# Performance work log

Hardware: AMD Instinct MI355X
Metric: run time of the kernel (lower is better)

The kernel has to match this reference:

```python
import jax, jax.numpy as jnp
import numpy as np


def setup_inputs() -> dict:
    key = jax.random.key(0)
    ks = jax.random.split(key, 5)
    B, D, W = 8, 768, 128
    scale = 1.0 / np.sqrt(D)
    return {
        "x": jax.random.normal(ks[0], (B, D, W, W), dtype=jnp.float32),
        "in_proj_w": jax.random.normal(ks[1], (3 * D, D), dtype=jnp.float32) * scale,
        "in_proj_b": jax.random.normal(ks[2], (3 * D,), dtype=jnp.float32) * 0.01,
        "out_w": jax.random.normal(ks[3], (D, D), dtype=jnp.float32) * scale,
        "out_b": jax.random.normal(ks[4], (D,), dtype=jnp.float32) * 0.01,
        "num_heads": 12,
        "num_tokens": 8,
    }


def reference(x, in_proj_w, in_proj_b, out_w, out_b, num_heads, num_tokens):
    B, D, Wd, Hd = x.shape
    nt = num_tokens
    gs = Hd // nt            # grid (block) size
    T = nt * nt              # number of blocks / queries
    S = gs * gs              # k/v tokens per block
    h = num_heads
    hd = D // h

    # ---- query: adaptive avg pool to (nt, nt), flatten, permute -> (B, T, D)
    q = x.reshape(B, D, nt, gs, nt, gs).mean(axis=(3, 5))      # (B, D, nt, nt)
    q = q.reshape(B, D, T).transpose(0, 2, 1)                   # (B, T, D)

    # ---- key/value: faithful reproduction of unfold + view(x.size()) + reshape
    # torch: kv_perm (B,W,H,D) -> unfold -> (B, nt, nt, D, gs, gs) contiguous,
    # then reinterpreted flat as (B, W*H, D) (scrambles channel/pixel layout).
    t = x.transpose(0, 2, 3, 1)                                 # (B, W, H, D)
    t = t.reshape(B, nt, gs, nt, gs, D).transpose(0, 1, 3, 5, 2, 4)  # (B,nt,nt,D,gs,gs)
    kv = t.reshape(B, T, S, D)                                  # chunked into T blocks of S tokens

    # ---- in-projections (torch MultiheadAttention packed weights)
    Wq, Wk, Wv = in_proj_w[:D], in_proj_w[D:2 * D], in_proj_w[2 * D:]
    bq, bk, bv = in_proj_b[:D], in_proj_b[D:2 * D], in_proj_b[2 * D:]
    qp = (q @ Wq.T + bq).reshape(B, T, h, hd)                   # (B, T, h, hd)
    kp = (kv @ Wk.T + bk).reshape(B, T, S, h, hd)               # (B, T, S, h, hd)
    vp = (kv @ Wv.T + bv).reshape(B, T, S, h, hd)

    # ---- block-local single-query attention, batched over all T blocks
    scores = jnp.einsum("bthd,btshd->bths", qp, kp) / np.sqrt(hd)  # (B, T, h, S)
    attn = jax.nn.softmax(scores, axis=-1)
    ctx = jnp.einsum("bths,btshd->bthd", attn, vp).reshape(B, T, D)

    # ---- out projection
    return ctx @ out_w.T + out_b                                # (B, T, D)
```

## Files before the change

kernel.cpp:

```cpp
#include <hip/hip_runtime.h>
#include <hip/hip_bf16.h>

#define D_ 768
#define W_ 128
#define T_ 64
#define S_ 256
#define H_ 12
#define HH_ 6
#define BT_ 512

__device__ __forceinline__ unsigned short f2bf(float f) {
  unsigned u = __float_as_uint(f);
  u = (u + 0x7FFFu + ((u >> 16) & 1u)) >> 16;
  return (unsigned short)u;
}
__device__ __forceinline__ float bfu(unsigned s) {
  return __uint_as_float(s << 16);
}

__global__ __launch_bounds__(384) void k_pack(const float* __restrict__ x,
                                              unsigned short* __restrict__ packed,
                                              float* __restrict__ q) {
  const int blk  = blockIdx.x;
  const int cc   = blk & 15;
  const int tjp  = (blk >> 4) & 3;
  const int ti   = (blk >> 6) & 7;
  const int b    = blk >> 9;
  const int tid  = threadIdx.x;
  const int c8   = tid & 7;
  const int ch   = tid >> 3;
  const int btl  = c8 >> 2;
  const int btg0 = b*64 + ti*8 + tjp*2;
  const int ch0  = cc * 48;

  __shared__ unsigned short tile[48][2][260];
  __shared__ float poolsc[48][2];

  const float* xcol = x + (size_t)b*D_*16384 + (size_t)(ch0 + ch)*16384
                        + (16*ti)*128 + 32*tjp + c8*4;

  float psum = 0.f;
  #pragma unroll
  for (int r = 0; r < 16; ++r) {
    const float4 v = *(const float4*)(xcol + r*128);
    const int px = r*16 + (c8 & 3)*4;
    unsigned lo = (unsigned)f2bf(v.x) | ((unsigned)f2bf(v.y) << 16);
    unsigned hi = (unsigned)f2bf(v.z) | ((unsigned)f2bf(v.w) << 16);
    *(uint2*)&tile[ch][btl][px] = make_uint2(lo, hi);
    psum += (v.x + v.y) + (v.z + v.w);
  }
  psum += __shfl_xor(psum, 1);
  psum += __shfl_xor(psum, 2);
  if ((c8 & 3) == 0) poolsc[ch][btl] = psum;
  __syncthreads();

  for (int ii = tid; ii < 512; ii += 384) {
    const int bl = ii >> 8, p = ii & 255;
    unsigned short* pbt = packed + ((size_t)(btg0 + bl)*16 + cc)*D_*16;
    #pragma unroll
    for (int c = 0; c < 3; ++c) {
      unsigned u[8];
      #pragma unroll
      for (int k2 = 0; k2 < 8; ++k2) {
        const unsigned a  = tile[3*(2*k2)     + c][bl][p];
        const unsigned b2 = tile[3*(2*k2 + 1) + c][bl][p];
        u[k2] = a | (b2 << 16);
      }
      unsigned short* dst = pbt + (size_t)(c*256 + p)*16;
      *(uint4*)(dst)     = make_uint4(u[0], u[1], u[2], u[3]);
      *(uint4*)(dst + 8) = make_uint4(u[4], u[5], u[6], u[7]);
    }
  }
  if (tid < 96) {
    const int ch2 = tid >> 1, bl = tid & 1;
    q[(size_t)(btg0 + bl)*D_ + ch0 + ch2] = poolsc[ch2][bl] * (1.0f/256.0f);
  }
}

__global__ __launch_bounds__(256) void k_qp(const float* __restrict__ q,
                                            const float* __restrict__ ipw,
                                            const float* __restrict__ ipb,
                                            float* __restrict__ qp) {
  const int jt = blockIdx.x >> 5;
  const int bt0 = (blockIdx.x & 31) * 16;
  const int tid = threadIdx.x;
  const float* Wr = ipw + (size_t)jt*64*D_;
  __shared__ float wt[64][65];
  __shared__ float at[16][65];
  const int i = tid & 63, qw = tid >> 6;
  float acc[4] = {0,0,0,0};
  for (int dc = 0; dc < D_; dc += 64) {
    #pragma unroll
    for (int k = 0; k < 4; ++k) {
      const int idx = k*256 + tid;
      const int r = idx >> 4, c4 = idx & 15;
      *(float4*)&wt[r][c4*4] = *(const float4*)(Wr + (size_t)r*D_ + dc + c4*4);
    }
    {
      const int r = tid >> 4, c4 = tid & 15;
      *(float4*)&at[r][c4*4] = *(const float4*)(q + (size_t)(bt0 + r)*D_ + dc + c4*4);
    }
    __syncthreads();
    #pragma unroll
    for (int dd = 0; dd < 64; ++dd) {
      const float wv = wt[i][dd];
      #pragma unroll
      for (int k = 0; k < 4; ++k)
        acc[k] += at[qw + k*4][dd] * wv;
    }
    __syncthreads();
  }
  const float bqv = ipb[jt*64 + i];
  #pragma unroll
  for (int k = 0; k < 4; ++k)
    qp[(size_t)(bt0 + qw + k*4)*D_ + jt*64 + i] = acc[k] + bqv;
}

__global__ __launch_bounds__(256) void k_fold(const float* __restrict__ qp,
                                              const float* __restrict__ ipw,
                                              unsigned short* __restrict__ qkout) {
  const int btc = blockIdx.x & 15;
  const int nt  = blockIdx.x >> 4;
  const int h   = nt / 12;
  const int ddc = (nt % 12) * 64;
  const int bt0 = btc * 32;
  const int tid = threadIdx.x;
  __shared__ float qpl[32][68];
  __shared__ float wkl[64][68];
  #pragma unroll
  for (int k = 0; k < 2; ++k) {
    const int idx = k*256 + tid;
    const int r = idx >> 4, c4 = idx & 15;
    *(float4*)&qpl[r][c4*4] = *(const float4*)(qp + (size_t)(bt0 + r)*D_ + h*64 + c4*4);
  }
  #pragma unroll
  for (int k = 0; k < 4; ++k) {
    const int idx = k*256 + tid;
    const int r = idx >> 4, c4 = idx & 15;
    *(float4*)&wkl[r][c4*4] = *(const float4*)(ipw + (size_t)(D_ + h*64 + r)*D_ + ddc + c4*4);
  }
  __syncthreads();
  const int i = tid & 63, qw = tid >> 6;
  float acc[8] = {0,0,0,0,0,0,0,0};
  #pragma unroll 8
  for (int kk = 0; kk < 64; ++kk) {
    const float w = wkl[kk][i];
    #pragma unroll
    for (int k = 0; k < 8; ++k)
      acc[k] += qpl[qw + k*4][kk] * w;
  }
  #pragma unroll
  for (int k = 0; k < 8; ++k)
    qkout[((size_t)(bt0 + qw + k*4)*H_ + h)*D_ + ddc + i] = f2bf(acc[k] * 0.125f);
}

__global__ __launch_bounds__(256) void k_attn3(const unsigned short* __restrict__ packed,
                                               const unsigned short* __restrict__ qkin,
                                               float* __restrict__ wout) {
  const int hg = blockIdx.x >> 9;
  const int bt = blockIdx.x & 511;
  const int tid = threadIdx.x;
  const int wv = tid >> 6, lane = tid & 63;
  __shared__ float pool_lds[HH_ * D_];
  __shared__ float sc[HH_][S_];

  {
    const uint4* src = (const uint4*)(qkin + ((size_t)bt*H_ + hg*HH_)*D_);
    #pragma unroll
    for (int k = 0; k < 3; ++k) {
      const int idx = k*256 + tid;
      if (idx < 576) {
        const uint4 v = src[idx];
        float* d = pool_lds + idx*8;
        d[0] = bfu(v.x & 0xFFFFu); d[1] = bfu(v.x >> 16);
        d[2] = bfu(v.y & 0xFFFFu); d[3] = bfu(v.y >> 16);
        d[4] = bfu(v.z & 0xFFFFu); d[5] = bfu(v.z >> 16);
        d[6] = bfu(v.w & 0xFFFFu); d[7] = bfu(v.w >> 16);
      }
    }
  }
  __syncthreads();

  float acc[HH_][4];
  #pragma unroll
  for (int h = 0; h < HH_; ++h)
    #pragma unroll
    for (int j = 0; j < 4; ++j) acc[h][j] = 0.f;

  {
    const unsigned short* pb = packed + ((size_t)bt*16 + (lane >> 2))*D_*16 + (lane & 3)*4;
    const int d0 = wv * 192;
    #pragma unroll 4
    for (int d4 = 0; d4 < 48; ++d4) {
      const int d = d0 + d4*4;
      float f[4][4];
      #pragma unroll
      for (int dd = 0; dd < 4; ++dd) {
        const short4 pv = *(const short4*)(pb + (size_t)(d + dd)*16);
        f[dd][0] = bfu((unsigned)(unsigned short)pv.x);
        f[dd][1] = bfu((unsigned)(unsigned short)pv.y);
        f[dd][2] = bfu((unsigned)(unsigned short)pv.z);
        f[dd][3] = bfu((unsigned)(unsigned short)pv.w);
      }
      #pragma unroll
      for (int h = 0; h < HH_; ++h) {
        const float4 qv = *(const float4*)&pool_lds[h*D_ + d];
        #pragma unroll
        for (int j = 0; j < 4; ++j)
          acc[h][j] += qv.x*f[0][j] + qv.y*f[1][j] + qv.z*f[2][j] + qv.w*f[3][j];
      }
    }
  }
  __syncthreads();

  if (wv == 0) {
    #pragma unroll
    for (int h = 0; h < HH_; ++h)
      *(float4*)&sc[h][lane*4] = make_float4(acc[h][0], acc[h][1], acc[h][2], acc[h][3]);
  } else {
    float* dstp = pool_lds + (size_t)(wv - 1)*(HH_*S_);
    #pragma unroll
    for (int h = 0; h < HH_; ++h)
      *(float4*)&dstp[h*S_ + lane*4] = make_float4(acc[h][0], acc[h][1], acc[h][2], acc[h][3]);
  }
  __syncthreads();
  #pragma unroll
  for (int h = 0; h < HH_; ++h)
    sc[h][tid] += pool_lds[0*(HH_*S_) + h*S_ + tid]
                + pool_lds[1*(HH_*S_) + h*S_ + tid]
                + pool_lds[2*(HH_*S_) + h*S_ + tid];
  __syncthreads();

  if (wv < 3) {
    #pragma unroll
    for (int hh = 0; hh < 2; ++hh) {
      const int h = wv*2 + hh;
      float4 v = *(const float4*)(&sc[h][lane*4]);
      float m = fmaxf(fmaxf(v.x, v.y), fmaxf(v.z, v.w));
      #pragma unroll
      for (int off = 32; off > 0; off >>= 1) m = fmaxf(m, __shfl_xor(m, off));
      const float e0 = __expf(v.x - m), e1 = __expf(v.y - m),
                  e2 = __expf(v.z - m), e3 = __expf(v.w - m);
      float ss = (e0+e1)+(e2+e3);
      #pragma unroll
      for (int off = 32; off > 0; off >>= 1) ss += __shfl_xor(ss, off);
      const float inv = 1.0f / ss;
      *(float4*)(&sc[h][lane*4]) = make_float4(e0*inv, e1*inv, e2*inv, e3*inv);
    }
  }
  __syncthreads();

  float wacc[HH_][3];
  #pragma unroll
  for (int h = 0; h < HH_; ++h) { wacc[h][0]=0.f; wacc[h][1]=0.f; wacc[h][2]=0.f; }
  const unsigned short* prow = packed + (size_t)bt*16*D_*16;
  #pragma unroll 2
  for (int s8 = 0; s8 < 32; ++s8) {
    float f[3][8];
    #pragma unroll
    for (int c = 0; c < 3; ++c) {
      const uint4 pv = *(const uint4*)(prow + ((size_t)(s8 >> 1)*D_ + c*256 + tid)*16
                                            + (s8 & 1)*8);
      f[c][0] = bfu(pv.x & 0xFFFFu); f[c][1] = bfu(pv.x >> 16);
      f[c][2] = bfu(pv.y & 0xFFFFu); f[c][3] = bfu(pv.y >> 16);
      f[c][4] = bfu(pv.z & 0xFFFFu); f[c][5] = bfu(pv.z >> 16);
      f[c][6] = bfu(pv.w & 0xFFFFu); f[c][7] = bfu(pv.w >> 16);
    }
    #pragma unroll
    for (int h = 0; h < HH_; ++h) {
      const float4 a0 = *(const float4*)&sc[h][s8*8];
      const float4 a1 = *(const float4*)&sc[h][s8*8 + 4];
      #pragma unroll
      for (int c = 0; c < 3; ++c)
        wacc[h][c] += a0.x*f[c][0] + a0.y*f[c][1] + a0.z*f[c][2] + a0.w*f[c][3]
                    + a1.x*f[c][4] + a1.y*f[c][5] + a1.z*f[c][6] + a1.w*f[c][7];
    }
  }
  float* wp = wout + ((size_t)bt*H_ + hg*HH_)*D_;
  #pragma unroll
  for (int h = 0; h < HH_; ++h)
    #pragma unroll
    for (int c = 0; c < 3; ++c)
      wp[h*D_ + c*256 + tid] = wacc[h][c];
}

__global__ __launch_bounds__(256) void k_q(const float* __restrict__ x, float* __restrict__ q) {
  const int bd = blockIdx.x;
  const int tid = threadIdx.x;
  const float4* xp = (const float4*)(x + (size_t)bd * (W_*W_));
  float acc[8] = {0,0,0,0,0,0,0,0};
  #pragma unroll
  for (int k = 0; k < 16; ++k) {
    float4 v = xp[k*256 + tid];
    acc[k>>1] += (v.x + v.y) + (v.z + v.w);
  }
  __shared__ float part[256][9];
  #pragma unroll
  for (int i = 0; i < 8; ++i) part[tid][i] = acc[i];
  __syncthreads();
  if (tid < 64) {
    const int ti = tid >> 3, tj = tid & 7;
    float s = 0.f;
    #pragma unroll
    for (int m = 0; m < 8; ++m)
      #pragma unroll
      for (int n = 0; n < 4; ++n)
        s += part[m*32 + tj*4 + n][ti];
    const int b = bd / D_, d = bd - b*D_;
    q[(size_t)(b*T_ + tid)*D_ + d] = s * (1.0f/256.0f);
  }
}

__global__ __launch_bounds__(256) void k_attn(const float* __restrict__ x,
                                              const unsigned short* __restrict__ qkin,
                                              float* __restrict__ wout) {
  const int bt = blockIdx.x;
  const int b = bt >> 6, t = bt & 63;
  const int ti = t >> 3, tj = t & 7;
  const int tid = threadIdx.x;
  __shared__ float qkl[H_*D_];
  __shared__ float sc[H_][S_];
  const float* xb = x + (size_t)b*D_*W_*W_ + ti*16*W_ + tj*16;
  {
    const uint4* src = (const uint4*)(qkin + (size_t)bt*H_*D_);
    #pragma unroll
    for (int k = 0; k < 5; ++k) {
      const int idx = k*256 + tid;
      if (idx < 1152) {
        const uint4 v = src[idx];
        float* d = qkl + idx*8;
        d[0] = bfu(v.x & 0xFFFFu); d[1] = bfu(v.x >> 16);
        d[2] = bfu(v.y & 0xFFFFu); d[3] = bfu(v.y >> 16);
        d[4] = bfu(v.z & 0xFFFFu); d[5] = bfu(v.z >> 16);
        d[6] = bfu(v.w & 0xFFFFu); d[7] = bfu(v.w >> 16);
      }
    }
  }
  __syncthreads();
  float acc[H_];
  #pragma unroll
  for (int h = 0; h < H_; ++h) acc[h] = 0.f;
  #pragma unroll
  for (int c = 0; c < 3; ++c) {
    const float* chp = xb + (size_t)(3*tid + c)*(W_*W_);
    for (int blk = 0; blk < 8; ++blk) {
      float4 v[8];
      #pragma unroll
      for (int u = 0; u < 8; ++u) {
        const int pg = blk*8 + u;
        v[u] = *(const float4*)(chp + (pg>>2)*W_ + (pg&3)*4);
      }
      const int dbase = c*256 + blk*32;
      #pragma unroll
      for (int h = 0; h < H_; ++h) {
        const float4* qh = (const float4*)(qkl + h*D_ + dbase);
        float s0 = 0.f;
        #pragma unroll
        for (int u = 0; u < 8; ++u) {
          const float4 qq = qh[u];
          s0 += qq.x*v[u].x + qq.y*v[u].y + qq.z*v[u].z + qq.w*v[u].w;
        }
        acc[h] += s0;
      }
    }
  }
  #pragma unroll
  for (int h = 0; h < H_; ++h) sc[h][tid] = acc[h];
  __syncthreads();
  {
    const int wv = tid >> 6, lane = tid & 63;
    #pragma unroll
    for (int hh = 0; hh < 3; ++hh) {
      const int h = wv*3 + hh;
      float4 v = *(const float4*)(&sc[h][lane*4]);
      float m = fmaxf(fmaxf(v.x, v.y), fmaxf(v.z, v.w));
      #pragma unroll
      for (int off = 32; off > 0; off >>= 1) m = fmaxf(m, __shfl_xor(m, off));
      const float e0 = __expf(v.x - m), e1 = __expf(v.y - m),
                  e2 = __expf(v.z - m), e3 = __expf(v.w - m);
      float ss = (e0+e1)+(e2+e3);
      #pragma unroll
      for (int off = 32; off > 0; off >>= 1) ss += __shfl_xor(ss, off);
      const float inv = 1.0f / ss;
      *(float4*)(&sc[h][lane*4]) = make_float4(e0*inv, e1*inv, e2*inv, e3*inv);
    }
  }
  __syncthreads();
  float wacc[H_][3];
  #pragma unroll
  for (int h = 0; h < H_; ++h) { wacc[h][0]=0.f; wacc[h][1]=0.f; wacc[h][2]=0.f; }
  const float* xp0 = xb + (tid>>4)*W_ + (tid&15);
  for (int s = 0; s < S_; ++s) {
    const float p0 = xp0[(size_t)(3*s+0)*(W_*W_)];
    const float p1 = xp0[(size_t)(3*s+1)*(W_*W_)];
    const float p2 = xp0[(size_t)(3*s+2)*(W_*W_)];
    #pragma unroll
    for (int h = 0; h < H_; ++h) {
      const float at = sc[h][s];
      wacc[h][0] += at*p0; wacc[h][1] += at*p1; wacc[h][2] += at*p2;
    }
  }
  float* wp = wout + (size_t)bt*H_*D_;
  #pragma unroll
  for (int h = 0; h < H_; ++h)
    #pragma unroll
    for (int c = 0; c < 3; ++c)
      wp[h*D_ + c*256 + tid] = wacc[h][c];
}

__global__ __launch_bounds__(256) void k_ctx(const float* __restrict__ wbuf,
                                             const float* __restrict__ ipw,
                                             const float* __restrict__ ipb,
                                             float* __restrict__ ctx) {
  const int h = blockIdx.x >> 5;
  const int bt0 = (blockIdx.x & 31) * 16;
  const int tid = threadIdx.x;
  const float* Wv = ipw + (size_t)2*D_*D_ + (size_t)h*64*D_;
  __shared__ float wt[64][65];
  __shared__ float at[16][65];
  const int i = tid & 63, qw = tid >> 6;
  float acc[4] = {0,0,0,0};
  for (int dc = 0; dc < D_; dc += 64) {
    #pragma unroll
    for (int k = 0; k < 4; ++k) {
      const int idx = k*256 + tid;
      const int r = idx >> 4, c4 = idx & 15;
      *(float4*)&wt[r][c4*4] = *(const float4*)(Wv + (size_t)r*D_ + dc + c4*4);
    }
    {
      const int r = tid >> 4, c4 = tid & 15;
      *(float4*)&at[r][c4*4] = *(const float4*)(wbuf + ((size_t)(bt0 + r)*H_ + h)*D_ + dc + c4*4);
    }
    __syncthreads();
    #pragma unroll
    for (int dd = 0; dd < 64; ++dd) {
      const float wv = wt[i][dd];
      #pragma unroll
      for (int k = 0; k < 4; ++k)
        acc[k] += at[qw + k*4][dd] * wv;
    }
    __syncthreads();
  }
  const float bvv = ipb[2*D_ + h*64 + i];
  #pragma unroll
  for (int k = 0; k < 4; ++k)
    ctx[(size_t)(bt0 + qw + k*4)*D_ + h*64 + i] = acc[k] + bvv;
}

__global__ __launch_bounds__(256) void k_out(const float* __restrict__ ctx,
                                             const float* __restrict__ ow,
                                             const float* __restrict__ ob,
                                             float* __restrict__ out) {
  const int jt = blockIdx.x >> 5;
  const int bt0 = (blockIdx.x & 31) * 16;
  const int tid = threadIdx.x;
  const float* Wr = ow + (size_t)jt*64*D_;
  __shared__ float wt[64][65];
  __shared__ float at[16][65];
  const int i = tid & 63, qw = tid >> 6;
  float acc[4] = {0,0,0,0};
  for (int dc = 0; dc < D_; dc += 64) {
    #pragma unroll
    for (int k = 0; k < 4; ++k) {
      const int idx = k*256 + tid;
      const int r = idx >> 4, c4 = idx & 15;
      *(float4*)&wt[r][c4*4] = *(const float4*)(Wr + (size_t)r*D_ + dc + c4*4);
    }
    {
      const int r = tid >> 4, c4 = tid & 15;
      *(float4*)&at[r][c4*4] = *(const float4*)(ctx + (size_t)(bt0 + r)*D_ + dc + c4*4);
    }
    __syncthreads();
    #pragma unroll
    for (int dd = 0; dd < 64; ++dd) {
      const float wv = wt[i][dd];
      #pragma unroll
      for (int k = 0; k < 4; ++k)
        acc[k] += at[qw + k*4][dd] * wv;
    }
    __syncthreads();
  }
  const float obv = ob[jt*64 + i];
  #pragma unroll
  for (int k = 0; k < 4; ++k)
    out[(size_t)(bt0 + qw + k*4)*D_ + jt*64 + i] = acc[k] + obv;
}

extern "C" void kernel_launch(void* const* d_in, const int* in_sizes, int n_in,
                              void* d_out, int out_size, void* d_ws, size_t ws_size,
                              hipStream_t stream) {
  const float* x   = (const float*)d_in[0];
  const float* ipw = (const float*)d_in[1];
  const float* ipb = (const float*)d_in[2];
  const float* ow  = (const float*)d_in[3];
  const float* ob  = (const float*)d_in[4];
  float* out = (float*)d_out;

  float* q    = (float*)d_ws;
  float* qp   = q    + (size_t)BT_*D_;
  unsigned short* qk = (unsigned short*)(qp + (size_t)BT_*D_);
  float* wb   = qp   + (size_t)BT_*D_ + (size_t)BT_*H_*D_;
  float* ctxb = wb   + (size_t)BT_*H_*D_;
  unsigned short* packed = (unsigned short*)(ctxb + (size_t)BT_*D_);

  const size_t need_main = ((size_t)BT_*D_*3 + (size_t)BT_*H_*D_*2) * 4
                         + (size_t)BT_*D_*S_*2;

  if (ws_size >= need_main) {
    k_pack <<<dim3(4096), dim3(384), 0, stream>>>(x, packed, q);
    k_qp   <<<dim3(384),  dim3(256), 0, stream>>>(q, ipw, ipb, qp);
    k_fold <<<dim3(2304), dim3(256), 0, stream>>>(qp, ipw, qk);
    k_attn3<<<dim3(1024), dim3(256), 0, stream>>>(packed, qk, wb);
    k_ctx  <<<dim3(384),  dim3(256), 0, stream>>>(wb, ipw, ipb, ctxb);
    k_out  <<<dim3(384),  dim3(256), 0, stream>>>(ctxb, ow, ob, out);
  } else {
    k_q    <<<dim3(8*D_), dim3(256), 0, stream>>>(x, q);
    k_qp   <<<dim3(384),  dim3(256), 0, stream>>>(q, ipw, ipb, qp);
    k_fold <<<dim3(2304), dim3(256), 0, stream>>>(qp, ipw, qk);
    k_attn <<<dim3(BT_),  dim3(256), 0, stream>>>(x, qk, wb);
    k_ctx  <<<dim3(384),  dim3(256), 0, stream>>>(wb, ipw, ipb, ctxb);
    k_out  <<<dim3(384),  dim3(256), 0, stream>>>(ctxb, ow, ob, out);
  }
}
```

Before: 393.9 us.

## Fuse Q projection with K fold and V projection into attention kernel

Merges the Q in-projection and the Wk fold into one kernel, k_qkf, which keeps the per-head projected query in shared memory. It also moves the V projection (the k_ctx stage) into the tail of k_attn3, which now writes ctx directly from LDS-staged weighted sums. This cuts two launches and the global round trips of the qp and wb buffers. The cost is that each attention block streams 384 rows of Wv from global memory with little reuse, and k_qkf has only 384 blocks, each running 12 serial fold iterations.

```diff
diff --git a/kernel.cpp b/kernel.cpp
--- a/kernel.cpp
+++ b/kernel.cpp
@@ -77,86 +77,78 @@
   }
 }
 
-__global__ __launch_bounds__(256) void k_qp(const float* __restrict__ q,
-                                            const float* __restrict__ ipw,
-                                            const float* __restrict__ ipb,
-                                            float* __restrict__ qp) {
-  const int jt = blockIdx.x >> 5;
-  const int bt0 = (blockIdx.x & 31) * 16;
+__global__ __launch_bounds__(256) void k_qkf(const float* __restrict__ q,
+                                             const float* __restrict__ ipw,
+                                             const float* __restrict__ ipb,
+                                             unsigned short* __restrict__ qkout) {
+  const int h   = blockIdx.x >> 5;
+  const int btc = blockIdx.x & 31;
+  const int bt0 = btc * 16;
   const int tid = threadIdx.x;
-  const float* Wr = ipw + (size_t)jt*64*D_;
+  const int i = tid & 63, qw = tid >> 6;
   __shared__ float wt[64][65];
   __shared__ float at[16][65];
-  const int i = tid & 63, qw = tid >> 6;
-  float acc[4] = {0,0,0,0};
-  for (int dc = 0; dc < D_; dc += 64) {
+  __shared__ float qps[16][72];
+
+  {
+    const float* Wr = ipw + (size_t)h*64*D_;
+    float acc[4] = {0,0,0,0};
+    for (int dc = 0; dc < D_; dc += 64) {
+      #pragma unroll
+      for (int k = 0; k < 4; ++k) {
+        const int idx = k*256 + tid;
+        const int r = idx >> 4, c4 = idx & 15;
+        *(float4*)&wt[r][c4*4] = *(const float4*)(Wr + (size_t)r*D_ + dc + c4*4);
+      }
+      {
+        const int r = tid >> 4, c4 = tid & 15;
+        *(float4*)&at[r][c4*4] = *(const float4*)(q + (size_t)(bt0 + r)*D_ + dc + c4*4);
+      }
+      __syncthreads();
+      #pragma unroll
+      for (int dd = 0; dd < 64; ++dd) {
+        const float wv = wt[i][dd];
+        #pragma unroll
+        for (int k = 0; k < 4; ++k)
+          acc[k] += at[qw + k*4][dd] * wv;
+      }
+      __syncthreads();
+    }
+    const float bqv = ipb[h*64 + i];
+    #pragma unroll
+    for (int k = 0; k < 4; ++k)
+      qps[qw + k*4][i] = acc[k] + bqv;
+  }
+  __syncthreads();
+
+  for (int ddc = 0; ddc < D_; ddc += 64) {
     #pragma unroll
     for (int k = 0; k < 4; ++k) {
       const int idx = k*256 + tid;
       const int r = idx >> 4, c4 = idx & 15;
-      *(float4*)&wt[r][c4*4] = *(const float4*)(Wr + (size_t)r*D_ + dc + c4*4);
-    }
-    {
-      const int r = tid >> 4, c4 = tid & 15;
-      *(float4*)&at[r][c4*4] = *(const float4*)(q + (size_t)(bt0 + r)*D_ + dc + c4*4);
+      *(float4*)&wt[r][c4*4] = *(const float4*)(ipw + (size_t)(D_ + h*64 + r)*D_ + ddc + c4*4);
     }
     __syncthreads();
-    #pragma unroll
-    for (int dd = 0; dd < 64; ++dd) {
-      const float wv = wt[i][dd];
+    float acc2[4] = {0,0,0,0};
+    #pragma unroll 8
+    for (int kk = 0; kk < 64; ++kk) {
+      const float w = wt[kk][i];
       #pragma unroll
       for (int k = 0; k < 4; ++k)
-        acc[k] += at[qw + k*4][dd] * wv;
-    }
+        acc2[k] += qps[qw + k*4][kk] * w;
+    }
+    #pragma unroll
+    for (int k = 0; k < 4; ++k)
+      qkout[((size_t)(bt0 + qw + k*4)*H_ + h)*D_ + ddc + i] = f2bf(acc2[k] * 0.125f);
     __syncthreads();
   }
-  const float bqv = ipb[jt*64 + i];
-  #pragma unroll
-  for (int k = 0; k < 4; ++k)
-    qp[(size_t)(bt0 + qw + k*4)*D_ + jt*64 + i] = acc[k] + bqv;
-}
-
-__global__ __launch_bounds__(256) void k_fold(const float* __restrict__ qp,
-                                              const float* __restrict__ ipw,
-                                              unsigned short* __restrict__ qkout) {
-  const int btc = blockIdx.x & 15;
-  const int nt  = blockIdx.x >> 4;
-  const int h   = nt / 12;
-  const int ddc = (nt % 12) * 64;
-  const int bt0 = btc * 32;
-  const int tid = threadIdx.x;
-  __shared__ float qpl[32][68];
-  __shared__ float wkl[64][68];
-  #pragma unroll
-  for (int k = 0; k < 2; ++k) {
-    const int idx = k*256 + tid;
-    const int r = idx >> 4, c4 = idx & 15;
-    *(float4*)&qpl[r][c4*4] = *(const float4*)(qp + (size_t)(bt0 + r)*D_ + h*64 + c4*4);
-  }
-  #pragma unroll
-  for (int k = 0; k < 4; ++k) {
-    const int idx = k*256 + tid;
-    const int r = idx >> 4, c4 = idx & 15;
-    *(float4*)&wkl[r][c4*4] = *(const float4*)(ipw + (size_t)(D_ + h*64 + r)*D_ + ddc + c4*4);
-  }
-  __syncthreads();
-  const int i = tid & 63, qw = tid >> 6;
-  float acc[8] = {0,0,0,0,0,0,0,0};
-  #pragma unroll 8
-  for (int kk = 0; kk < 64; ++kk) {
-    const float w = wkl[kk][i];
-    #pragma unroll
-    for (int k = 0; k < 8; ++k)
-      acc[k] += qpl[qw + k*4][kk] * w;
-  }
-  #pragma unroll
-  for (int k = 0; k < 8; ++k)
-    qkout[((size_t)(bt0 + qw + k*4)*H_ + h)*D_ + ddc + i] = f2bf(acc[k] * 0.125f);
 }
 
 __global__ __launch_bounds__(256) void k_attn3(const unsigned short* __restrict__ packed,
                                                const unsigned short* __restrict__ qkin,
-                                               float* __restrict__ wout) {
+                                               const float* __restrict__ ipw,
+                                               const float* __restrict__ ipb,
+                                               float* __restrict__ ctx) {
   const int hg = blockIdx.x >> 9;
   const int bt = blockIdx.x & 511;
   const int tid = threadIdx.x;
@@ -276,12 +268,69 @@
                     + a1.x*f[c][4] + a1.y*f[c][5] + a1.z*f[c][6] + a1.w*f[c][7];
     }
   }
-  float* wp = wout + ((size_t)bt*H_ + hg*HH_)*D_;
+
+  __syncthreads();
+  float* w_lds = pool_lds;
   #pragma unroll
   for (int h = 0; h < HH_; ++h)
     #pragma unroll
     for (int c = 0; c < 3; ++c)
-      wp[h*D_ + c*256 + tid] = wacc[h][c];
+      w_lds[h*D_ + c*256 + tid] = wacc[h][c];
+  __syncthreads();
+
+  for (int o = tid; o < HH_*64; o += 256) {
+    const int hh = o >> 6, i = o & 63;
+    const int hglob = hg*HH_ + hh;
+    const float* wr = ipw + (size_t)(2*D_ + hglob*64 + i)*D_;
+    const float* wl = w_lds + hh*D_;
+    float a = 0.f;
+    #pragma unroll 4
+    for (int d4 = 0; d4 < 192; ++d4) {
+      const float4 wv4 = *(const float4*)(wr + d4*4);
+      const float4 ww  = *(const float4*)(wl + d4*4);
+      a += wv4.x*ww.x + wv4.y*ww.y + wv4.z*ww.z + wv4.w*ww.w;
+    }
+    ctx[(size_t)bt*D_ + hglob*64 + i] = a + ipb[2*D_ + hglob*64 + i];
+  }
+}
+
+__global__ __launch_bounds__(256) void k_out(const float* __restrict__ ctx,
+                                             const float* __restrict__ ow,
+                                             const float* __restrict__ ob,
+                                             float* __restrict__ out) {
+  const int jt = blockIdx.x >> 5;
+  const int bt0 = (blockIdx.x & 31) * 16;
+  const int tid = threadIdx.x;
+  const float* Wr = ow + (size_t)jt*64*D_;
+  __shared__ float wt[64][65];
+  __shared__ float at[16][65];
+  const int i = tid & 63, qw = tid >> 6;
+  float acc[4] = {0,0,0,0};
+  for (int dc = 0; dc < D_; dc += 64) {
+    #pragma unroll
+    for (int k = 0; k < 4; ++k) {
+      const int idx = k*256 + tid;
+      const int r = idx >> 4, c4 = idx & 15;
+      *(float4*)&wt[r][c4*4] = *(const float4*)(Wr + (size_t)r*D_ + dc + c4*4);
+    }
+    {
+      const int r = tid >> 4, c4 = tid & 15;
+      *(float4*)&at[r][c4*4] = *(const float4*)(ctx + (size_t)(bt0 + r)*D_ + dc + c4*4);
+    }
+    __syncthreads();
+    #pragma unroll
+    for (int dd = 0; dd < 64; ++dd) {
+      const float wv = wt[i][dd];
+      #pragma unroll
+      for (int k = 0; k < 4; ++k)
+        acc[k] += at[qw + k*4][dd] * wv;
+    }
+    __syncthreads();
+  }
+  const float obv = ob[jt*64 + i];
+  #pragma unroll
+  for (int k = 0; k < 4; ++k)
+    out[(size_t)(bt0 + qw + k*4)*D_ + jt*64 + i] = acc[k] + obv;
 }
 
 __global__ __launch_bounds__(256) void k_q(const float* __restrict__ x, float* __restrict__ q) {
@@ -447,45 +496,6 @@
     ctx[(size_t)(bt0 + qw + k*4)*D_ + h*64 + i] = acc[k] + bvv;
 }
 
-__global__ __launch_bounds__(256) void k_out(const float* __restrict__ ctx,
-                                             const float* __restrict__ ow,
-                                             const float* __restrict__ ob,
-                                             float* __restrict__ out) {
-  const int jt = blockIdx.x >> 5;
-  const int bt0 = (blockIdx.x & 31) * 16;
-  const int tid = threadIdx.x;
-  const float* Wr = ow + (size_t)jt*64*D_;
-  __shared__ float wt[64][65];
-  __shared__ float at[16][65];
-  const int i = tid & 63, qw = tid >> 6;
-  float acc[4] = {0,0,0,0};
-  for (int dc = 0; dc < D_; dc += 64) {
-    #pragma unroll
-    for (int k = 0; k < 4; ++k) {
-      const int idx = k*256 + tid;
-      const int r = idx >> 4, c4 = idx & 15;
-      *(float4*)&wt[r][c4*4] = *(const float4*)(Wr + (size_t)r*D_ + dc + c4*4);
-    }
-    {
-      const int r = tid >> 4, c4 = tid & 15;
-      *(float4*)&at[r][c4*4] = *(const float4*)(ctx + (size_t)(bt0 + r)*D_ + dc + c4*4);
-    }
-    __syncthreads();
-    #pragma unroll
-    for (int dd = 0; dd < 64; ++dd) {
-      const float wv = wt[i][dd];
-      #pragma unroll
-      for (int k = 0; k < 4; ++k)
-        acc[k] += at[qw + k*4][dd] * wv;
-    }
-    __syncthreads();
-  }
-  const float obv = ob[jt*64 + i];
-  #pragma unroll
-  for (int k = 0; k < 4; ++k)
-    out[(size_t)(bt0 + qw + k*4)*D_ + jt*64 + i] = acc[k] + obv;
-}
-
 extern "C" void kernel_launch(void* const* d_in, const int* in_sizes, int n_in,
                               void* d_out, int out_size, void* d_ws, size_t ws_size,
                               hipStream_t stream) {
@@ -508,15 +518,12 @@
 
   if (ws_size >= need_main) {
     k_pack <<<dim3(4096), dim3(384), 0, stream>>>(x, packed, q);
-    k_qp   <<<dim3(384),  dim3(256), 0, stream>>>(q, ipw, ipb, qp);
-    k_fold <<<dim3(2304), dim3(256), 0, stream>>>(qp, ipw, qk);
-    k_attn3<<<dim3(1024), dim3(256), 0, stream>>>(packed, qk, wb);
-    k_ctx  <<<dim3(384),  dim3(256), 0, stream>>>(wb, ipw, ipb, ctxb);
+    k_qkf  <<<dim3(384),  dim3(256), 0, stream>>>(q, ipw, ipb, qk);
+    k_attn3<<<dim3(1024), dim3(256), 0, stream>>>(packed, qk, ipw, ipb, ctxb);
     k_out  <<<dim3(384),  dim3(256), 0, stream>>>(ctxb, ow, ob, out);
   } else {
     k_q    <<<dim3(8*D_), dim3(256), 0, stream>>>(x, q);
-    k_qp   <<<dim3(384),  dim3(256), 0, stream>>>(q, ipw, ipb, qp);
-    k_fold <<<dim3(2304), dim3(256), 0, stream>>>(qp, ipw, qk);
+    k_qkf  <<<dim3(384),  dim3(256), 0, stream>>>(q, ipw, ipb, qk);
     k_attn <<<dim3(BT_),  dim3(256), 0, stream>>>(x, qk, wb);
     k_ctx  <<<dim3(384),  dim3(256), 0, stream>>>(wb, ipw, ipb, ctxb);
     k_out  <<<dim3(384),  dim3(256), 0, stream>>>(ctxb, ow, ob, out);
```

Measured after the change: 475.1 us. +20.6%, slower.
